# Performance work log

Measured on AMD Instinct MI355X. Metric: run time of the kernel, lower is better.

## Reference

```python
import jax, jax.numpy as jnp
import numpy as np

N_NODES = 50000
N_EDGES = 800000
D_IN = 64
D_OUT = 64
D_HID = 64
EPS = 1e-5


def _init_params(key):
    ks = jax.random.split(key, 12)
    s = 0.05
    p = {}
    p["W_lin"] = jax.random.normal(ks[0], (D_IN, D_OUT), jnp.float32) * s
    p["W_src"] = jax.random.normal(ks[1], (D_IN, D_OUT), jnp.float32) * s
    p["W_dst"] = jax.random.normal(ks[2], (D_IN, D_OUT), jnp.float32) * s
    p["pos_w1"] = jax.random.normal(ks[3], (3, D_HID), jnp.float32) * s
    p["pos_b1"] = jnp.zeros((D_HID,), jnp.float32)
    p["pos_w2"] = jax.random.normal(ks[4], (D_HID, D_OUT), jnp.float32) * s
    p["pos_b2"] = jnp.zeros((D_OUT,), jnp.float32)
    p["attn_w1"] = jax.random.normal(ks[5], (D_OUT, D_HID), jnp.float32) * s
    p["attn_b1"] = jnp.zeros((D_HID,), jnp.float32)
    p["attn_w2"] = jax.random.normal(ks[6], (D_HID, D_OUT), jnp.float32) * s
    p["attn_b2"] = jnp.zeros((D_OUT,), jnp.float32)
    p["gamma"] = jnp.ones((D_OUT,), jnp.float32)
    p["beta"] = jnp.zeros((D_OUT,), jnp.float32)
    return p


def setup_inputs() -> dict:
    key = jax.random.key(0)
    k1, k2, k3, k4 = jax.random.split(key, 4)
    inp = {
        "x": jax.random.normal(k1, (N_NODES, D_IN), jnp.float32),
        "pos": jax.random.normal(k2, (N_NODES, 3), jnp.float32),
        "edge_index": jax.random.randint(k3, (2, N_EDGES), 0, N_NODES, jnp.int64),
    }
    inp.update(_init_params(k4))
    return inp


def _segment_softmax(alpha, seg, num_segments):
    # channel-wise softmax over edges sharing the same destination node
    m = jax.ops.segment_max(alpha, seg, num_segments=num_segments)  # [N, D]
    e = jnp.exp(alpha - m[seg])
    z = jax.ops.segment_sum(e, seg, num_segments=num_segments)  # [N, D]
    return e / (z[seg] + 1e-16)


def reference(x, pos, edge_index, W_lin, W_src, W_dst,
              pos_w1, pos_b1, pos_w2, pos_b2,
              attn_w1, attn_b1, attn_w2, attn_b2, gamma, beta):
    N = x.shape[0]
    # add self loops (PointTransformerConv default add_self_loops=True)
    loops = jnp.arange(N, dtype=edge_index.dtype)
    src = jnp.concatenate([edge_index[0], loops])  # j
    dst = jnp.concatenate([edge_index[1], loops])  # i (aggregation target)

    x_val = x @ W_lin          # [N, D] value projection
    a_src = x @ W_src          # alpha_j source term
    a_dst = x @ W_dst          # alpha_i destination term

    # per-edge positional encoding: pos_nn(pos_i - pos_j), two Linears, no activation
    rel = pos[dst] - pos[src]                         # [E, 3]
    delta = (rel @ pos_w1 + pos_b1) @ pos_w2 + pos_b2  # [E, D]

    # attention logits: attn_nn(alpha_i - alpha_j + delta)
    alpha = a_dst[dst] - a_src[src] + delta
    alpha = (alpha @ attn_w1 + attn_b1) @ attn_w2 + attn_b2  # [E, D]
    alpha = _segment_softmax(alpha, dst, N)

    # message and scatter-sum aggregation
    msg = alpha * (x_val[src] + delta)                # [E, D]
    out = jax.ops.segment_sum(msg, dst, num_segments=N)  # [N, D]

    out = jax.nn.elu(out)

    # BatchNorm over nodes (training-mode batch stats, biased var, eps=1e-5)
    mean = jnp.mean(out, axis=0)
    var = jnp.var(out, axis=0)
    out = (out - mean) * jax.lax.rsqrt(var + EPS) * gamma + beta
    return out
```

## Files before the change

kernel.cpp:

```cpp
#include <hip/hip_runtime.h>
#include <cmath>


__device__ __forceinline__ unsigned bf16r(float f) {
    unsigned u = __float_as_uint(f);
    return (u + 0x7fffu + ((u >> 16) & 1u)) >> 16;
}
__device__ __forceinline__ float bfhi(unsigned u) { return __uint_as_float(u & 0xffff0000u); }
__device__ __forceinline__ float bflo(unsigned u) { return __uint_as_float(u << 16); }

__device__ __forceinline__ void gemm_tile(const float (*xs)[68], const float (*Wl)[64],
                                          int tx, int ty, float acc[4][4])
{
    #pragma unroll
    for (int i = 0; i < 4; ++i)
        #pragma unroll
        for (int j = 0; j < 4; ++j) acc[i][j] = 0.f;
    for (int k = 0; k < 64; k += 4) {
        float4 b0 = *(const float4*)&Wl[k + 0][4 * tx];
        float4 b1 = *(const float4*)&Wl[k + 1][4 * tx];
        float4 b2 = *(const float4*)&Wl[k + 2][4 * tx];
        float4 b3 = *(const float4*)&Wl[k + 3][4 * tx];
        #pragma unroll
        for (int i = 0; i < 4; ++i) {
            float4 a = *(const float4*)&xs[4 * ty + i][k];
            acc[i][0] += a.x * b0.x + a.y * b1.x + a.z * b2.x + a.w * b3.x;
            acc[i][1] += a.x * b0.y + a.y * b1.y + a.z * b2.y + a.w * b3.y;
            acc[i][2] += a.x * b0.z + a.y * b1.z + a.z * b2.z + a.w * b3.z;
            acc[i][3] += a.x * b0.w + a.y * b1.w + a.z * b2.w + a.w * b3.w;
        }
    }
}

__global__ __launch_bounds__(256) void k_pre1(
    const float* __restrict__ attn_w1, const float* __restrict__ attn_w2,
    const float* __restrict__ pos_w1, const float* __restrict__ pos_b1,
    const float* __restrict__ pos_w2, const float* __restrict__ pos_b2,
    float* __restrict__ A2, float* __restrict__ M3, float* __restrict__ bc,
    int* __restrict__ cnt, float* __restrict__ stats, int n_nodes)
{
    int t = threadIdx.x;
    if (blockIdx.x == 0) {
        __shared__ __align__(16) float As[64][68];
        __shared__ __align__(16) float Bs[64][64];
        int lk = t & 63, lr = t >> 6;
        for (int i = 0; i < 16; ++i) {
            As[lr + 4 * i][lk] = attn_w1[(lr + 4 * i) * 64 + lk];
            Bs[lr + 4 * i][lk] = attn_w2[(lr + 4 * i) * 64 + lk];
        }
        __syncthreads();
        int tx = t & 15, ty = t >> 4;
        float acc[4][4];
        gemm_tile(As, Bs, tx, ty, acc);
        #pragma unroll
        for (int i = 0; i < 4; ++i)
            *(float4*)&A2[(4 * ty + i) * 64 + 4 * tx] =
                make_float4(acc[i][0], acc[i][1], acc[i][2], acc[i][3]);
    } else if (blockIdx.x == 1) {
        int c = t & 63, q = t >> 6;
        if (q < 3) {
            float acc = 0.f;
            for (int h = 0; h < 64; ++h) acc += pos_w1[q * 64 + h] * pos_w2[h * 64 + c];
            M3[q * 64 + c] = acc;
        } else {
            float accb = 0.f;
            for (int h = 0; h < 64; ++h) accb += pos_b1[h] * pos_w2[h * 64 + c];
            bc[c] = accb + pos_b2[c];
        }
    } else {
        if (blockIdx.x == 2 && t < 128) stats[t] = 0.f;
        int idx = (blockIdx.x - 2) * 256 + t;
        int stride = (gridDim.x - 2) * 256;
        for (int i = idx; i < n_nodes; i += stride) cnt[i] = 0;
    }
}

__global__ __launch_bounds__(256) void k_pre2(
    const float* __restrict__ W_src, const float* __restrict__ A2,
    const float* __restrict__ M3,
    float* __restrict__ Wsrc2, float* __restrict__ M5)
{
    int t = threadIdx.x;
    if (blockIdx.x == 0) {
        __shared__ __align__(16) float As[64][68];
        __shared__ __align__(16) float Bs[64][64];
        int lk = t & 63, lr = t >> 6;
        for (int i = 0; i < 16; ++i) {
            As[lr + 4 * i][lk] = W_src[(lr + 4 * i) * 64 + lk];
            Bs[lr + 4 * i][lk] = A2[(lr + 4 * i) * 64 + lk];
        }
        __syncthreads();
        int tx = t & 15, ty = t >> 4;
        float acc[4][4];
        gemm_tile(As, Bs, tx, ty, acc);
        #pragma unroll
        for (int i = 0; i < 4; ++i)
            *(float4*)&Wsrc2[(4 * ty + i) * 64 + 4 * tx] =
                make_float4(acc[i][0], acc[i][1], acc[i][2], acc[i][3]);
    } else {
        int c = t & 63, q = t >> 6;
        if (q < 3) {
            float acc = 0.f;
            for (int k = 0; k < 64; ++k) acc += M3[q * 64 + k] * A2[k * 64 + c];
            M5[q * 64 + c] = acc;
        }
    }
}

__global__ __launch_bounds__(256, 4) void k_gemm_pair_hist(
    const float* __restrict__ x, const float* __restrict__ pos,
    const float* __restrict__ Wsrc2, const float* __restrict__ Wlin,
    const float* __restrict__ M3, const float* __restrict__ M5,
    unsigned* __restrict__ pairbf, int n_nodes,
    const int* __restrict__ ei, int* __restrict__ cnt, int n_edges, int G)
{
    int t = threadIdx.x;
    if ((int)blockIdx.x >= G) {
        int idx = ((int)blockIdx.x - G) * 256 + t;
        int stride = ((int)gridDim.x - G) * 256;
        for (int i = idx; i < n_edges; i += stride)
            atomicAdd(&cnt[ei[n_edges + i]], 1);
        return;
    }
    __shared__ __align__(16) float xs[64][68];
    __shared__ __align__(16) float Wl[64][64];
    __shared__ float ps[192];
    __shared__ float m3s[192], m5s[192];
    int tx = t & 15;
    int ty = t >> 4;
    int nbase = blockIdx.x * 64;
    int lk = t & 63;
    int lr = t >> 6;

    for (int i = 0; i < 16; ++i) {
        int n = lr + 4 * i;
        int gn = nbase + n;
        xs[n][lk] = (gn < n_nodes) ? x[gn * 64 + lk] : 0.f;
    }
    if (t < 192) {
        int gi = nbase * 3 + t;
        ps[t] = (gi < n_nodes * 3) ? pos[gi] : 0.f;
        m3s[t] = M3[t];
        m5s[t] = M5[t];
    }
    for (int i = 0; i < 16; ++i) Wl[lr + 4 * i][lk] = Wsrc2[(lr + 4 * i) * 64 + lk];
    __syncthreads();

    float acc_s[4][4];
    gemm_tile(xs, Wl, tx, ty, acc_s);

    __syncthreads();
    for (int i = 0; i < 16; ++i) Wl[lr + 4 * i][lk] = Wlin[(lr + 4 * i) * 64 + lk];
    __syncthreads();

    float acc_x[4][4];
    gemm_tile(xs, Wl, tx, ty, acc_x);

    #pragma unroll
    for (int i = 0; i < 4; ++i) {
        int n = 4 * ty + i;
        int gn = nbase + n;
        if (gn < n_nodes) {
            float px = ps[3 * n], py = ps[3 * n + 1], pz = ps[3 * n + 2];
            int c0 = 4 * tx;
            float g50 = px * m5s[c0]     + py * m5s[64 + c0]     + pz * m5s[128 + c0];
            float g51 = px * m5s[c0 + 1] + py * m5s[64 + c0 + 1] + pz * m5s[128 + c0 + 1];
            float g52 = px * m5s[c0 + 2] + py * m5s[64 + c0 + 2] + pz * m5s[128 + c0 + 2];
            float g53 = px * m5s[c0 + 3] + py * m5s[64 + c0 + 3] + pz * m5s[128 + c0 + 3];
            float g30 = px * m3s[c0]     + py * m3s[64 + c0]     + pz * m3s[128 + c0];
            float g31 = px * m3s[c0 + 1] + py * m3s[64 + c0 + 1] + pz * m3s[128 + c0 + 1];
            float g32 = px * m3s[c0 + 2] + py * m3s[64 + c0 + 2] + pz * m3s[128 + c0 + 2];
            float g33 = px * m3s[c0 + 3] + py * m3s[64 + c0 + 3] + pz * m3s[128 + c0 + 3];
            uint4 w;
            w.x = (bf16r(__expf(-(acc_s[i][0] + g50))) << 16) | bf16r(acc_x[i][0] - g30);
            w.y = (bf16r(__expf(-(acc_s[i][1] + g51))) << 16) | bf16r(acc_x[i][1] - g31);
            w.z = (bf16r(__expf(-(acc_s[i][2] + g52))) << 16) | bf16r(acc_x[i][2] - g32);
            w.w = (bf16r(__expf(-(acc_s[i][3] + g53))) << 16) | bf16r(acc_x[i][3] - g33);
            *(uint4*)&pairbf[gn * 64 + c0] = w;
        }
    }
}

#define SCAN_CHUNK 4096

__global__ __launch_bounds__(256) void k_scan_partial(const int* __restrict__ cnt,
                                                      int* __restrict__ bsum, int n)
{
    __shared__ int wsh[4];
    int b = blockIdx.x, t = threadIdx.x;
    int base = b * SCAN_CHUNK + t * 16;
    int s = 0;
    #pragma unroll
    for (int i = 0; i < 16; ++i) {
        int idx = base + i;
        if (idx < n) s += cnt[idx];
    }
    for (int off = 32; off; off >>= 1) s += __shfl_down(s, off, 64);
    int lane = t & 63, wv = t >> 6;
    if (lane == 0) wsh[wv] = s;
    __syncthreads();
    if (t == 0) bsum[b] = wsh[0] + wsh[1] + wsh[2] + wsh[3];
}

__global__ __launch_bounds__(256) void k_scan_final(const int* __restrict__ cnt,
                                                    const int* __restrict__ bsum,
                                                    int* __restrict__ rowptr,
                                                    int* __restrict__ cursor,
                                                    int n, int nch, int n_edges)
{
    __shared__ int wsh[4];
    __shared__ int bb;
    int b = blockIdx.x, t = threadIdx.x;
    if (t == 0) {
        int acc = 0;
        for (int c = 0; c < b; ++c) acc += bsum[c];
        bb = acc;
        if (b == nch - 1) rowptr[n] = n_edges;
    }
    int base = b * SCAN_CHUNK + t * 16;
    int v[16];
    int s = 0;
    #pragma unroll
    for (int i = 0; i < 16; ++i) {
        int idx = base + i;
        v[i] = (idx < n) ? cnt[idx] : 0;
        s += v[i];
    }
    int lane = t & 63, wv = t >> 6;
    int inc = s;
    for (int off = 1; off < 64; off <<= 1) {
        int u = __shfl_up(inc, off, 64);
        if (lane >= off) inc += u;
    }
    if (lane == 63) wsh[wv] = inc;
    __syncthreads();
    if (t == 0) {
        int acc = 0;
        for (int w = 0; w < 4; ++w) { int tmp = wsh[w]; wsh[w] = acc; acc += tmp; }
    }
    __syncthreads();
    int run = bb + wsh[wv] + inc - s;
    #pragma unroll
    for (int i = 0; i < 16; ++i) {
        int idx = base + i;
        if (idx < n) {
            rowptr[idx] = run;
            cursor[idx] = run;
            run += v[i];
        }
    }
}

__global__ __launch_bounds__(256) void k_scatter(const int* __restrict__ ei,
                                                 int* __restrict__ cursor,
                                                 int* __restrict__ csr_src,
                                                 int n_edges)
{
    int i = blockIdx.x * blockDim.x + threadIdx.x;
    if (i < n_edges) {
        int dst = ei[n_edges + i];
        int p = atomicAdd(&cursor[dst], 1);
        csr_src[p] = ei[i] * 64;
    }
}

__global__ __launch_bounds__(256) void k_gather(
    const int* __restrict__ rowptr, const int* __restrict__ csr_src,
    const unsigned* __restrict__ pairbf, const float* __restrict__ pos,
    const float* __restrict__ M3, const float* __restrict__ bc,
    float* __restrict__ out, float* __restrict__ stats, int n_nodes)
{
    int t = threadIdx.x;
    int c = t & 63;
    float bcc = bc[c];
    float m30 = M3[c], m31 = M3[64 + c], m32 = M3[128 + c];

    int wid = (blockIdx.x * blockDim.x + t) >> 6;
    int nw = (gridDim.x * blockDim.x) >> 6;

    float lsum = 0.f, lsq = 0.f;

    for (int i = wid; i < n_nodes; i += nw) {
        int beg = rowptr[i], end = rowptr[i + 1];
        float px = pos[3 * i], py = pos[3 * i + 1], pz = pos[3 * i + 2];
        float ddi = bcc + px * m30 + py * m31 + pz * m32;
        unsigned up = pairbf[i * 64 + c];
        float w = bfhi(up);
        float zz = w;
        float SS = w * bflo(up);

        int k = beg;
        for (; k + 8 <= end; k += 8) {
            int s0 = csr_src[k],     s1 = csr_src[k + 1];
            int s2 = csr_src[k + 2], s3 = csr_src[k + 3];
            int s4 = csr_src[k + 4], s5 = csr_src[k + 5];
            int s6 = csr_src[k + 6], s7 = csr_src[k + 7];
            unsigned u0 = pairbf[s0 + c], u1 = pairbf[s1 + c];
            unsigned u2 = pairbf[s2 + c], u3 = pairbf[s3 + c];
            unsigned u4 = pairbf[s4 + c], u5 = pairbf[s5 + c];
            unsigned u6 = pairbf[s6 + c], u7 = pairbf[s7 + c];
            float w0 = bfhi(u0), w1 = bfhi(u1), w2 = bfhi(u2), w3 = bfhi(u3);
            float w4 = bfhi(u4), w5 = bfhi(u5), w6 = bfhi(u6), w7 = bfhi(u7);
            zz += ((w0 + w1) + (w2 + w3)) + ((w4 + w5) + (w6 + w7));
            SS += w0 * bflo(u0) + w1 * bflo(u1) + w2 * bflo(u2) + w3 * bflo(u3)
                + w4 * bflo(u4) + w5 * bflo(u5) + w6 * bflo(u6) + w7 * bflo(u7);
        }
        for (; k < end; ++k) {
            unsigned u0 = pairbf[csr_src[k] + c];
            float w0 = bfhi(u0);
            zz += w0;
            SS += w0 * bflo(u0);
        }

        float v = SS / zz + ddi;
        v = (v > 0.f) ? v : expm1f(v);
        out[i * 64 + c] = v;
        lsum += v;
        lsq += v * v;
    }

    __shared__ float sred[256], sred2[256];
    sred[t] = lsum;
    sred2[t] = lsq;
    __syncthreads();
    if (t < 64) {
        float s = sred[t] + sred[t + 64] + sred[t + 128] + sred[t + 192];
        float q = sred2[t] + sred2[t + 64] + sred2[t + 128] + sred2[t + 192];
        unsafeAtomicAdd(&stats[t], s);
        unsafeAtomicAdd(&stats[64 + t], q);
    }
}

__global__ __launch_bounds__(256) void k_bn(
    float4* __restrict__ out4, const float* __restrict__ stats,
    const float* __restrict__ gamma, const float* __restrict__ beta,
    int total4, float inv_n)
{
    __shared__ float ssc[64], ssh[64];
    int t = threadIdx.x;
    if (t < 64) {
        float mean = stats[t] * inv_n;
        float var = stats[64 + t] * inv_n - mean * mean;
        float scale = (1.0f / sqrtf(var + 1e-5f)) * gamma[t];
        ssc[t] = scale;
        ssh[t] = beta[t] - mean * scale;
    }
    __syncthreads();
    for (int idx = blockIdx.x * blockDim.x + t; idx < total4;
         idx += gridDim.x * blockDim.x) {
        float4 v = out4[idx];
        int c0 = (idx << 2) & 63;
        v.x = v.x * ssc[c0]     + ssh[c0];
        v.y = v.y * ssc[c0 + 1] + ssh[c0 + 1];
        v.z = v.z * ssc[c0 + 2] + ssh[c0 + 2];
        v.w = v.w * ssc[c0 + 3] + ssh[c0 + 3];
        out4[idx] = v;
    }
}

extern "C" void kernel_launch(void* const* d_in, const int* in_sizes, int n_in,
                              void* d_out, int out_size, void* d_ws, size_t ws_size,
                              hipStream_t stream)
{
    const float* x        = (const float*)d_in[0];
    const float* pos      = (const float*)d_in[1];
    const int*   ei       = (const int*)d_in[2];
    const float* W_lin    = (const float*)d_in[3];
    const float* W_src    = (const float*)d_in[4];
    const float* pos_w1   = (const float*)d_in[6];
    const float* pos_b1   = (const float*)d_in[7];
    const float* pos_w2   = (const float*)d_in[8];
    const float* pos_b2   = (const float*)d_in[9];
    const float* attn_w1  = (const float*)d_in[10];
    const float* attn_w2  = (const float*)d_in[12];
    const float* gamma    = (const float*)d_in[14];
    const float* beta     = (const float*)d_in[15];

    int n_nodes = in_sizes[0] / 64;
    int n_edges = in_sizes[2] / 2;
    int total = n_nodes * 64;
    int nch = (n_nodes + SCAN_CHUNK - 1) / SCAN_CHUNK;

    unsigned* pairbf = (unsigned*)d_ws;
    float* A2    = (float*)(pairbf + total);
    float* Wsrc2 = A2 + 4096;
    float* M3    = Wsrc2 + 4096;
    float* M5    = M3 + 192;
    float* bc    = M5 + 192;
    float* stats = bc + 64;
    int*   cnt     = (int*)(stats + 128);
    int*   rowptr  = cnt + n_nodes;
    int*   cursor  = rowptr + n_nodes + 1;
    int*   csr_src = cursor + n_nodes;
    int*   bsum    = csr_src + n_edges;

    int G = (n_nodes + 63) / 64;

    k_pre1<<<18, 256, 0, stream>>>(attn_w1, attn_w2, pos_w1, pos_b1, pos_w2,
                                   pos_b2, A2, M3, bc, cnt, stats, n_nodes);
    k_pre2<<<2, 256, 0, stream>>>(W_src, A2, M3, Wsrc2, M5);
    k_gemm_pair_hist<<<G + 512, 256, 0, stream>>>(
        x, pos, Wsrc2, W_lin, M3, M5, pairbf, n_nodes, ei, cnt, n_edges, G);
    k_scan_partial<<<nch, 256, 0, stream>>>(cnt, bsum, n_nodes);
    k_scan_final<<<nch, 256, 0, stream>>>(cnt, bsum, rowptr, cursor,
                                          n_nodes, nch, n_edges);
    k_scatter<<<(n_edges + 255) / 256, 256, 0, stream>>>(ei, cursor, csr_src, n_edges);
    k_gather<<<2048, 256, 0, stream>>>(rowptr, csr_src, pairbf, pos, M3, bc,
                                       (float*)d_out, stats, n_nodes);
    k_bn<<<2048, 256, 0, stream>>>((float4*)d_out, stats, gamma, beta, total / 4,
                                   1.0f / (float)n_nodes);
}
```

Measured before the change: 203.6 us.

## Split pair table into four channel-quarter planes and gather four edges per wave

The packed bf16 pair table is reorganized into four planes of 16 channels each, and the gather kernel processes one plane at a time with each wave covering 4 edges in parallel (16 lanes per edge), then reducing across lane groups with shuffles. The aim is to shrink the working set of each pass so the gathered rows stay in cache, and to raise memory-level parallelism on low-degree nodes. The cost is that rowptr, csr_src and pos are read four times, each 64-byte gather is narrower, and extra shuffles and block reductions are added.

```diff
diff --git a/kernel.cpp b/kernel.cpp
--- a/kernel.cpp
+++ b/kernel.cpp
@@ -111,7 +111,7 @@
     const float* __restrict__ x, const float* __restrict__ pos,
     const float* __restrict__ Wsrc2, const float* __restrict__ Wlin,
     const float* __restrict__ M3, const float* __restrict__ M5,
-    unsigned* __restrict__ pairbf, int n_nodes,
+    unsigned* __restrict__ pairq, int n_nodes,
     const int* __restrict__ ei, int* __restrict__ cnt, int n_edges, int G)
 {
     int t = threadIdx.x;
@@ -131,6 +131,7 @@
     int nbase = blockIdx.x * 64;
     int lk = t & 63;
     int lr = t >> 6;
+    int n16 = n_nodes * 16;
 
     for (int i = 0; i < 16; ++i) {
         int n = lr + 4 * i;
@@ -176,7 +177,7 @@
             w.y = (bf16r(__expf(-(acc_s[i][1] + g51))) << 16) | bf16r(acc_x[i][1] - g31);
             w.z = (bf16r(__expf(-(acc_s[i][2] + g52))) << 16) | bf16r(acc_x[i][2] - g32);
             w.w = (bf16r(__expf(-(acc_s[i][3] + g53))) << 16) | bf16r(acc_x[i][3] - g33);
-            *(uint4*)&pairbf[gn * 64 + c0] = w;
+            *(uint4*)&pairq[(c0 >> 4) * n16 + gn * 16 + (c0 & 15)] = w;
         }
     }
 }
@@ -260,74 +261,99 @@
     if (i < n_edges) {
         int dst = ei[n_edges + i];
         int p = atomicAdd(&cursor[dst], 1);
-        csr_src[p] = ei[i] * 64;
-    }
-}
-
-__global__ __launch_bounds__(256) void k_gather(
+        csr_src[p] = ei[i] * 16;
+    }
+}
+
+__global__ __launch_bounds__(256) void k_gather4(
     const int* __restrict__ rowptr, const int* __restrict__ csr_src,
-    const unsigned* __restrict__ pairbf, const float* __restrict__ pos,
+    const unsigned* __restrict__ pairq, const float* __restrict__ pos,
     const float* __restrict__ M3, const float* __restrict__ bc,
     float* __restrict__ out, float* __restrict__ stats, int n_nodes)
 {
     int t = threadIdx.x;
-    int c = t & 63;
-    float bcc = bc[c];
-    float m30 = M3[c], m31 = M3[64 + c], m32 = M3[128 + c];
+    int lane = t & 63;
+    int c = lane & 15;
+    int eg = lane >> 4;
+    int n16 = n_nodes * 16;
 
     int wid = (blockIdx.x * blockDim.x + t) >> 6;
     int nw = (gridDim.x * blockDim.x) >> 6;
 
-    float lsum = 0.f, lsq = 0.f;
-
-    for (int i = wid; i < n_nodes; i += nw) {
-        int beg = rowptr[i], end = rowptr[i + 1];
-        float px = pos[3 * i], py = pos[3 * i + 1], pz = pos[3 * i + 2];
-        float ddi = bcc + px * m30 + py * m31 + pz * m32;
-        unsigned up = pairbf[i * 64 + c];
-        float w = bfhi(up);
-        float zz = w;
-        float SS = w * bflo(up);
-
-        int k = beg;
-        for (; k + 8 <= end; k += 8) {
-            int s0 = csr_src[k],     s1 = csr_src[k + 1];
-            int s2 = csr_src[k + 2], s3 = csr_src[k + 3];
-            int s4 = csr_src[k + 4], s5 = csr_src[k + 5];
-            int s6 = csr_src[k + 6], s7 = csr_src[k + 7];
-            unsigned u0 = pairbf[s0 + c], u1 = pairbf[s1 + c];
-            unsigned u2 = pairbf[s2 + c], u3 = pairbf[s3 + c];
-            unsigned u4 = pairbf[s4 + c], u5 = pairbf[s5 + c];
-            unsigned u6 = pairbf[s6 + c], u7 = pairbf[s7 + c];
-            float w0 = bfhi(u0), w1 = bfhi(u1), w2 = bfhi(u2), w3 = bfhi(u3);
-            float w4 = bfhi(u4), w5 = bfhi(u5), w6 = bfhi(u6), w7 = bfhi(u7);
-            zz += ((w0 + w1) + (w2 + w3)) + ((w4 + w5) + (w6 + w7));
-            SS += w0 * bflo(u0) + w1 * bflo(u1) + w2 * bflo(u2) + w3 * bflo(u3)
-                + w4 * bflo(u4) + w5 * bflo(u5) + w6 * bflo(u6) + w7 * bflo(u7);
-        }
-        for (; k < end; ++k) {
-            unsigned u0 = pairbf[csr_src[k] + c];
-            float w0 = bfhi(u0);
-            zz += w0;
-            SS += w0 * bflo(u0);
-        }
-
-        float v = SS / zz + ddi;
-        v = (v > 0.f) ? v : expm1f(v);
-        out[i * 64 + c] = v;
-        lsum += v;
-        lsq += v * v;
+    float lsum[4], lsq[4];
+    #pragma unroll
+    for (int q = 0; q < 4; ++q) { lsum[q] = 0.f; lsq[q] = 0.f; }
+
+    #pragma unroll
+    for (int q = 0; q < 4; ++q) {
+        int ch = q * 16 + c;
+        float bcc = bc[ch];
+        float m30 = M3[ch], m31 = M3[64 + ch], m32 = M3[128 + ch];
+        const unsigned* __restrict__ base = pairq + q * n16;
+
+        for (int i = wid; i < n_nodes; i += nw) {
+            int beg = rowptr[i], end = rowptr[i + 1];
+            float px = pos[3 * i], py = pos[3 * i + 1], pz = pos[3 * i + 2];
+            float ddi = bcc + px * m30 + py * m31 + pz * m32;
+            unsigned up = base[i * 16 + c];
+            float ws = bfhi(up);
+            float zz = (eg == 0) ? ws : 0.f;
+            float SS = (eg == 0) ? ws * bflo(up) : 0.f;
+            float zzB = 0.f, SSB = 0.f;
+
+            int k = beg;
+            for (; k + 8 <= end; k += 8) {
+                int iA = csr_src[k + eg];
+                int iB = csr_src[k + 4 + eg];
+                unsigned uA = base[iA + c];
+                unsigned uB = base[iB + c];
+                float wA = bfhi(uA), wB = bfhi(uB);
+                zz += wA;  SS += wA * bflo(uA);
+                zzB += wB; SSB += wB * bflo(uB);
+            }
+            int r = end - k;
+            if (eg < r) {
+                int iA = csr_src[k + eg];
+                unsigned uA = base[iA + c];
+                float wA = bfhi(uA);
+                zz += wA; SS += wA * bflo(uA);
+            }
+            if (eg + 4 < r) {
+                int iB = csr_src[k + 4 + eg];
+                unsigned uB = base[iB + c];
+                float wB = bfhi(uB);
+                zzB += wB; SSB += wB * bflo(uB);
+            }
+            zz += zzB; SS += SSB;
+            zz += __shfl_xor(zz, 16, 64);
+            SS += __shfl_xor(SS, 16, 64);
+            zz += __shfl_xor(zz, 32, 64);
+            SS += __shfl_xor(SS, 32, 64);
+
+            float v = SS / zz + ddi;
+            v = (v > 0.f) ? v : expm1f(v);
+            if (eg == 0) {
+                out[i * 64 + ch] = v;
+                lsum[q] += v;
+                lsq[q] += v * v;
+            }
+        }
     }
 
     __shared__ float sred[256], sred2[256];
-    sred[t] = lsum;
-    sred2[t] = lsq;
-    __syncthreads();
-    if (t < 64) {
-        float s = sred[t] + sred[t + 64] + sred[t + 128] + sred[t + 192];
-        float q = sred2[t] + sred2[t + 64] + sred2[t + 128] + sred2[t + 192];
-        unsafeAtomicAdd(&stats[t], s);
-        unsafeAtomicAdd(&stats[64 + t], q);
+    #pragma unroll
+    for (int q = 0; q < 4; ++q) {
+        __syncthreads();
+        sred[t] = lsum[q];
+        sred2[t] = lsq[q];
+        __syncthreads();
+        if (t < 16) {
+            float s = 0.f, sq = 0.f;
+            #pragma unroll
+            for (int j = 0; j < 16; ++j) { s += sred[t + 16 * j]; sq += sred2[t + 16 * j]; }
+            unsafeAtomicAdd(&stats[q * 16 + t], s);
+            unsafeAtomicAdd(&stats[64 + q * 16 + t], sq);
+        }
     }
 }
 
@@ -381,8 +407,8 @@
     int total = n_nodes * 64;
     int nch = (n_nodes + SCAN_CHUNK - 1) / SCAN_CHUNK;
 
-    unsigned* pairbf = (unsigned*)d_ws;
-    float* A2    = (float*)(pairbf + total);
+    unsigned* pairq = (unsigned*)d_ws;
+    float* A2    = (float*)(pairq + total);
     float* Wsrc2 = A2 + 4096;
     float* M3    = Wsrc2 + 4096;
     float* M5    = M3 + 192;
@@ -400,13 +426,13 @@
                                    pos_b2, A2, M3, bc, cnt, stats, n_nodes);
     k_pre2<<<2, 256, 0, stream>>>(W_src, A2, M3, Wsrc2, M5);
     k_gemm_pair_hist<<<G + 512, 256, 0, stream>>>(
-        x, pos, Wsrc2, W_lin, M3, M5, pairbf, n_nodes, ei, cnt, n_edges, G);
+        x, pos, Wsrc2, W_lin, M3, M5, pairq, n_nodes, ei, cnt, n_edges, G);
     k_scan_partial<<<nch, 256, 0, stream>>>(cnt, bsum, n_nodes);
     k_scan_final<<<nch, 256, 0, stream>>>(cnt, bsum, rowptr, cursor,
                                           n_nodes, nch, n_edges);
     k_scatter<<<(n_edges + 255) / 256, 256, 0, stream>>>(ei, cursor, csr_src, n_edges);
-    k_gather<<<2048, 256, 0, stream>>>(rowptr, csr_src, pairbf, pos, M3, bc,
-                                       (float*)d_out, stats, n_nodes);
+    k_gather4<<<2048, 256, 0, stream>>>(rowptr, csr_src, pairq, pos, M3, bc,
+                                        (float*)d_out, stats, n_nodes);
     k_bn<<<2048, 256, 0, stream>>>((float4*)d_out, stats, gamma, beta, total / 4,
                                    1.0f / (float)n_nodes);
 }
```

New measurement: 230.0 us. +13.0%, slower.
